# Optimization experiments

Measured on AMD Instinct MI355X. Metric: run time of the kernel, lower is better.

The kernel has to match this reference:

```python
import jax, jax.numpy as jnp
import numpy as np
import math

B, T, V, D, H = 64, 128, 25, 256, 8
HD = D // H  # head_dim = 32
LN_EPS = 1e-5
NORM_EPS = 1e-12  # F.normalize default eps


def _layernorm(x, g, b):
    m = jnp.mean(x, axis=-1, keepdims=True)
    v = jnp.mean(jnp.square(x - m), axis=-1, keepdims=True)
    return (x - m) * jax.lax.rsqrt(v + LN_EPS) * g + b


def setup_inputs() -> dict:
    key = jax.random.key(0)
    ks = jax.random.split(key, 10)
    s = 0.02
    return {
        "x": jax.random.normal(ks[0], (B, T, V, D), dtype=jnp.float32),
        "ln1_g": jnp.ones((D,), jnp.float32),
        "ln1_b": jnp.zeros((D,), jnp.float32),
        "qkv_w": jax.random.normal(ks[1], (D, 3 * D), jnp.float32) * s,
        "qkv_b": jnp.zeros((3 * D,), jnp.float32),
        "proj_w": jax.random.normal(ks[2], (D, D), jnp.float32) * s,
        "proj_b": jnp.zeros((D,), jnp.float32),
        "logit_scale": jnp.full((H, 1, 1), math.log(math.sqrt(HD)), jnp.float32),
        "ln2_g": jnp.ones((D,), jnp.float32),
        "ln2_b": jnp.zeros((D,), jnp.float32),
        "ffn_w1": jax.random.normal(ks[3], (D, 4 * D), jnp.float32) * s,
        "ffn_b1": jnp.zeros((4 * D,), jnp.float32),
        "ffn_w2": jax.random.normal(ks[4], (4 * D, D), jnp.float32) * s,
        "ffn_b2": jnp.zeros((D,), jnp.float32),
    }


def reference(x, ln1_g, ln1_b, qkv_w, qkv_b, proj_w, proj_b, logit_scale,
              ln2_g, ln2_b, ffn_w1, ffn_b1, ffn_w2, ffn_b2):
    b, t, v, dm = x.shape
    n = b * t
    h, d = H, HD
    xf = x.reshape(n, v, dm)
    residual = xf
    y = _layernorm(xf, ln1_g, ln1_b)
    qkv = (y @ qkv_w + qkv_b).reshape(n, v, 3, h, d)
    qkv = jnp.transpose(qkv, (2, 0, 3, 1, 4))  # (3, n, h, v, d)
    q, k, val = qkv[0], qkv[1], qkv[2]
    # cosine attention: L2-normalize q/k, learned per-head temperature (clamped at 100)
    scale = jnp.exp(jnp.minimum(logit_scale, math.log(100.0)))  # (h,1,1)
    q = q / jnp.maximum(jnp.linalg.norm(q, axis=-1, keepdims=True), NORM_EPS) * scale[None]
    k = k / jnp.maximum(jnp.linalg.norm(k, axis=-1, keepdims=True), NORM_EPS)
    # SDPA applies its default 1/sqrt(head_dim) scaling on top
    logits = jnp.einsum('nhqd,nhkd->nhqk', q, k) / math.sqrt(d)
    attn = jax.nn.softmax(logits, axis=-1)
    out = jnp.einsum('nhqk,nhkd->nhqd', attn, val)
    out = jnp.transpose(out, (0, 2, 1, 3)).reshape(n, v, dm)
    out = out @ proj_w + proj_b
    xf = residual + out
    y2 = _layernorm(xf, ln2_g, ln2_b)
    ffn = jax.nn.gelu(y2 @ ffn_w1 + ffn_b1, approximate=False) @ ffn_w2 + ffn_b2
    xf = xf + ffn
    return xf.reshape(b, t, v, dm)
```

## Files before the change

### kernel.cpp

```cpp
#include <hip/hip_runtime.h>
#include <stdint.h>

typedef unsigned short u16;
typedef __attribute__((ext_vector_type(8))) short short8;
typedef __attribute__((ext_vector_type(4))) float f32x4;

__device__ __forceinline__ float bf2f(u16 v) {
  union { uint32_t u; float f; } x; x.u = ((uint32_t)v) << 16; return x.f;
}
__device__ __forceinline__ u16 f2bf(float f) {
  union { float f; uint32_t u; } x; x.f = f;
  uint32_t u = x.u;
  return (u16)((u + 0x7fffu + ((u >> 16) & 1u)) >> 16);
}
__device__ __forceinline__ void unp8(int4 r, float* f) {
  f[0] = __uint_as_float(((uint32_t)r.x) << 16);
  f[1] = __uint_as_float(((uint32_t)r.x) & 0xffff0000u);
  f[2] = __uint_as_float(((uint32_t)r.y) << 16);
  f[3] = __uint_as_float(((uint32_t)r.y) & 0xffff0000u);
  f[4] = __uint_as_float(((uint32_t)r.z) << 16);
  f[5] = __uint_as_float(((uint32_t)r.z) & 0xffff0000u);
  f[6] = __uint_as_float(((uint32_t)r.w) << 16);
  f[7] = __uint_as_float(((uint32_t)r.w) & 0xffff0000u);
}

__device__ __forceinline__ void copy16(const u16* g, u16* l) {
#if defined(__has_builtin) && __has_builtin(__builtin_amdgcn_global_load_lds)
  uintptr_t li = (uintptr_t)l;
  uintptr_t gi = (uintptr_t)g;
  __builtin_amdgcn_global_load_lds((const __attribute__((address_space(1))) uint32_t*)gi,
                                   (__attribute__((address_space(3))) uint32_t*)li, 16, 0, 0);
#else
  *(int4*)l = *(const int4*)g;
#endif
}

__global__ __launch_bounds__(256) void k0_prep(const float* __restrict__ qkvw,
                                               const float* __restrict__ projw,
                                               const float* __restrict__ w1,
                                               const float* __restrict__ w2,
                                               u16* __restrict__ wbuf) {
  int idx = blockIdx.x * 256 + threadIdx.x;
  if (idx < 196608) {
    int nn = idx >> 8, kk = idx & 255;
    wbuf[idx] = f2bf(qkvw[kk * 768 + nn]);
  } else if (idx < 262144) {
    int i = idx - 196608; int nn = i >> 8, kk = i & 255;
    wbuf[idx] = f2bf(projw[kk * 256 + nn]);
  } else if (idx < 524288) {
    int i = idx - 262144; int nn = i >> 8, kk = i & 255;
    wbuf[idx] = f2bf(w1[kk * 1024 + nn]);
  } else {
    int i = idx - 524288; int nn = i >> 10, kk = i & 1023;
    wbuf[idx] = f2bf(w2[kk * 256 + nn]);
  }
}

__global__ __launch_bounds__(256) void k1_ln1(const float* __restrict__ x,
                                              const float* __restrict__ g,
                                              const float* __restrict__ b,
                                              u16* __restrict__ Y, int row0) {
  int t = threadIdx.x; int lr = t >> 6; int lane = t & 63;
  size_t row = (size_t)blockIdx.x * 4 + lr;
  const float4 xv = *(const float4*)&x[((size_t)row0 + row) * 256 + lane * 4];
  float s = xv.x + xv.y + xv.z + xv.w;
  float q = xv.x * xv.x + xv.y * xv.y + xv.z * xv.z + xv.w * xv.w;
  #pragma unroll
  for (int off = 32; off > 0; off >>= 1) { s += __shfl_xor(s, off); q += __shfl_xor(q, off); }
  float mean = s * (1.0f / 256.0f);
  float var  = q * (1.0f / 256.0f) - mean * mean;
  float rstd = rsqrtf(var + 1e-5f);
  const float4 gv = *(const float4*)&g[lane * 4];
  const float4 bv = *(const float4*)&b[lane * 4];
  float y0 = (xv.x - mean) * rstd * gv.x + bv.x;
  float y1 = (xv.y - mean) * rstd * gv.y + bv.y;
  float y2 = (xv.z - mean) * rstd * gv.z + bv.z;
  float y3 = (xv.w - mean) * rstd * gv.w + bv.w;
  uint2 r;
  r.x = (uint32_t)f2bf(y0) | ((uint32_t)f2bf(y1) << 16);
  r.y = (uint32_t)f2bf(y2) | ((uint32_t)f2bf(y3) << 16);
  *(uint2*)&Y[row * 256 + lane * 4] = r;
}

template <int NB, bool GELU>
__global__ __launch_bounds__(256) void kA_gemm(const u16* __restrict__ A, const u16* __restrict__ Bw,
                                               const float* __restrict__ bias, u16* __restrict__ C) {
  __shared__ u16 Al[64 * 264];
  __shared__ u16 Bl[128 * 32];
  const int t = threadIdx.x, w = t >> 6, lane = t & 63, quad = lane >> 4, lrow = lane & 15;
  const int wm = w >> 1, wn = w & 1;
  const int mb = blockIdx.x * 64;
  #pragma unroll
  for (int r = 0; r < 8; r++) {
    int c = r * 256 + t;
    int row = c >> 5, col = (c & 31) * 8;
    int4 v = *(const int4*)&A[(size_t)(mb + row) * 256 + col];
    *(int4*)&Al[row * 264 + col] = v;
  }
  constexpr int LDC = NB * 128;
  for (int nb = 0; nb < NB; nb++) {
    f32x4 acc[2][4];
    #pragma unroll
    for (int i = 0; i < 2; i++)
      #pragma unroll
      for (int j = 0; j < 4; j++) acc[i][j] = f32x4{0.f, 0.f, 0.f, 0.f};
    for (int kc = 0; kc < 8; kc++) {
      #pragma unroll
      for (int r = 0; r < 2; r++) {
        int c = r * 256 + w * 64 + lane;
        u16* lp = Bl + (size_t)(r * 256 + w * 64) * 8;
        const u16* gp = Bw + (size_t)(nb * 128 + (c >> 2)) * 256 + kc * 32 + (c & 3) * 8;
        copy16(gp, lp);
      }
      __syncthreads();
      short8 af[2], bfr[4];
      #pragma unroll
      for (int mt = 0; mt < 2; mt++)
        af[mt] = *(const short8*)&Al[(wm * 32 + mt * 16 + lrow) * 264 + kc * 32 + quad * 8];
      #pragma unroll
      for (int nt = 0; nt < 4; nt++)
        bfr[nt] = *(const short8*)&Bl[(wn * 64 + nt * 16 + lrow) * 32 + quad * 8];
      #pragma unroll
      for (int mt = 0; mt < 2; mt++)
        #pragma unroll
        for (int nt = 0; nt < 4; nt++)
          acc[mt][nt] = __builtin_amdgcn_mfma_f32_16x16x32_bf16(af[mt], bfr[nt], acc[mt][nt], 0, 0, 0);
      __syncthreads();
    }
    #pragma unroll
    for (int nt = 0; nt < 4; nt++) {
      int n = nb * 128 + wn * 64 + nt * 16 + lrow;
      float bv = bias[n];
      #pragma unroll
      for (int mt = 0; mt < 2; mt++)
        #pragma unroll
        for (int i = 0; i < 4; i++) {
          int m = mb + wm * 32 + mt * 16 + quad * 4 + i;
          float u = acc[mt][nt][i] + bv;
          if (GELU) u = 0.5f * u * (1.0f + erff(u * 0.70710678118654752440f));
          C[(size_t)m * LDC + n] = f2bf(u);
        }
    }
  }
}

__global__ __launch_bounds__(256) void k3_attn(const u16* __restrict__ QKV,
                                               const float* __restrict__ lscale,
                                               u16* __restrict__ O) {
  __shared__ u16 Kl[8192];
  __shared__ u16 Vt[10304];
  __shared__ u16 Pl[4][1280];
  __shared__ float invk[256];

  const int n = blockIdx.x;
  const int t = threadIdx.x;
  const int w = t >> 6, lane = t & 63, quad = lane >> 4, l15 = lane & 15;
  const size_t n25 = (size_t)n * 25;

  #pragma unroll
  for (int r = 0; r < 4; r++) {
    int c = r * 256 + t;
    if (c < 800) {
      int vr = c >> 5, ci = c & 31;
      const u16* gp = QKV + (n25 + vr) * 768 + 256 + (size_t)((ci ^ (vr & 7)) * 8);
      u16* lp = Kl + (size_t)(r * 256 + w * 64) * 8;
      copy16(gp, lp);
    }
  }
  #pragma unroll
  for (int r = 0; r < 4; r++) {
    int c = r * 256 + t;
    if (c < 800) {
      int vr = c >> 5, ci = c & 31, h = ci >> 2, d8 = (ci & 3) * 8;
      int4 rv = *(const int4*)&QKV[(n25 + vr) * 768 + 512 + ci * 8];
      int base = h * 1288 + d8 * 40 + vr;
      Vt[base +   0] = (u16)((uint32_t)rv.x & 0xffffu);
      Vt[base +  40] = (u16)((uint32_t)rv.x >> 16);
      Vt[base +  80] = (u16)((uint32_t)rv.y & 0xffffu);
      Vt[base + 120] = (u16)((uint32_t)rv.y >> 16);
      Vt[base + 160] = (u16)((uint32_t)rv.z & 0xffffu);
      Vt[base + 200] = (u16)((uint32_t)rv.z >> 16);
      Vt[base + 240] = (u16)((uint32_t)rv.w & 0xffffu);
      Vt[base + 280] = (u16)((uint32_t)rv.w >> 16);
    }
  }
  {
    int h = t >> 5, d = t & 31;
    int base = h * 1288 + d * 40 + 25;
    #pragma unroll
    for (int j = 0; j < 7; j++) Vt[base + j] = 0;
  }
  __syncthreads();

  if (t < 200) {
    int h = (t * 41) >> 10;
    int vr = t - h * 25;
    float ss = 0.f;
    #pragma unroll
    for (int q = 0; q < 4; q++) {
      int chunk = (h * 4 + q) ^ (vr & 7);
      int4 rv = *(const int4*)&Kl[vr * 256 + chunk * 8];
      float f[8]; unp8(rv, f);
      #pragma unroll
      for (int j = 0; j < 8; j++) ss += f[j] * f[j];
    }
    invk[h * 32 + vr] = 1.0f / fmaxf(sqrtf(ss), 1e-12f);
  } else {
    int u = t - 200;
    int h = (u * 37) >> 8;
    int j = u - h * 7;
    invk[h * 32 + 25 + j] = 0.f;
  }
  __syncthreads();

  const u16* qbase = QKV + n25 * 768;
  const f32x4 zz = {0.f, 0.f, 0.f, 0.f};
  #pragma unroll
  for (int hh = 0; hh < 2; hh++) {
    const int h = w * 2 + hh;
    const float sc = expf(fminf(lscale[h], 4.6051701859880913680f));

    short8 af0 = *(const short8*)(qbase + (size_t)l15 * 768 + h * 32 + quad * 8);
    short8 af1 = *(const short8*)(qbase + (size_t)(16 + l15) * 768 + h * 32 + quad * 8);
    short8 bf0 = *(const short8*)&Kl[l15 * 256 + (((h * 4 + quad) ^ (l15 & 7)) * 8)];
    short8 bf1 = *(const short8*)&Kl[(16 + l15) * 256 + (((h * 4 + quad) ^ ((16 + l15) & 7)) * 8)];
    f32x4 sA[2][2];
    sA[0][0] = __builtin_amdgcn_mfma_f32_16x16x32_bf16(af0, bf0, zz, 0, 0, 0);
    sA[0][1] = __builtin_amdgcn_mfma_f32_16x16x32_bf16(af0, bf1, zz, 0, 0, 0);
    sA[1][0] = __builtin_amdgcn_mfma_f32_16x16x32_bf16(af1, bf0, zz, 0, 0, 0);
    sA[1][1] = __builtin_amdgcn_mfma_f32_16x16x32_bf16(af1, bf1, zz, 0, 0, 0);

    float ss0 = 0.f, ss1 = 0.f;
    #pragma unroll
    for (int j = 0; j < 8; j++) {
      float f0 = bf2f((u16)af0[j]); ss0 += f0 * f0;
      float f1 = bf2f((u16)af1[j]); ss1 += f1 * f1;
    }
    ss0 += __shfl_xor(ss0, 16); ss0 += __shfl_xor(ss0, 32);
    ss1 += __shfl_xor(ss1, 16); ss1 += __shfl_xor(ss1, 32);
    float fct0 = sc / (fmaxf(sqrtf(ss0), 1e-12f) * 5.6568542494923802f);
    float fct1 = sc / (fmaxf(sqrtf(ss1), 1e-12f) * 5.6568542494923802f);

    const float ik0 = invk[h * 32 + l15];
    const float ik1 = invk[h * 32 + 16 + l15];
    const bool v1 = l15 < 9;

    #pragma unroll
    for (int qt = 0; qt < 2; qt++) {
      #pragma unroll
      for (int i = 0; i < 4; i++) {
        float fr = __shfl(qt == 0 ? fct0 : fct1, quad * 4 + i);
        float l0 = sA[qt][0][i] * fr * ik0;
        float l1 = sA[qt][1][i] * fr * ik1;
        float m = fmaxf(l0, v1 ? l1 : -1e30f);
        #pragma unroll
        for (int o = 1; o < 16; o <<= 1) m = fmaxf(m, __shfl_xor(m, o));
        float e0 = expf(l0 - m);
        float e1 = v1 ? expf(l1 - m) : 0.f;
        float se = e0 + e1;
        #pragma unroll
        for (int o = 1; o < 16; o <<= 1) se += __shfl_xor(se, o);
        float inv = 1.0f / se;
        int q = qt * 16 + quad * 4 + i;
        Pl[w][q * 40 + l15]      = f2bf(e0 * inv);
        Pl[w][q * 40 + 16 + l15] = f2bf(e1 * inv);
      }
    }

    short8 pa0 = *(const short8*)&Pl[w][l15 * 40 + quad * 8];
    short8 pa1 = *(const short8*)&Pl[w][(16 + l15) * 40 + quad * 8];
    short8 vb0 = *(const short8*)&Vt[h * 1288 + l15 * 40 + quad * 8];
    short8 vb1 = *(const short8*)&Vt[h * 1288 + (16 + l15) * 40 + quad * 8];
    f32x4 oA[2][2];
    oA[0][0] = __builtin_amdgcn_mfma_f32_16x16x32_bf16(pa0, vb0, zz, 0, 0, 0);
    oA[0][1] = __builtin_amdgcn_mfma_f32_16x16x32_bf16(pa0, vb1, zz, 0, 0, 0);
    oA[1][0] = __builtin_amdgcn_mfma_f32_16x16x32_bf16(pa1, vb0, zz, 0, 0, 0);
    oA[1][1] = __builtin_amdgcn_mfma_f32_16x16x32_bf16(pa1, vb1, zz, 0, 0, 0);

    u16* ob = O + n25 * 256 + h * 32;
    #pragma unroll
    for (int qt = 0; qt < 2; qt++)
      #pragma unroll
      for (int i = 0; i < 4; i++) {
        int qr = quad * 4 + i;
        if (qt == 1 && qr >= 9) continue;
        int q = qt * 16 + qr;
        ob[(size_t)q * 256 + l15]      = f2bf(oA[qt][0][i]);
        ob[(size_t)q * 256 + 16 + l15] = f2bf(oA[qt][1][i]);
      }
  }
}

template <int BM, int BN>
__device__ __forceinline__ void gemm_core(const u16* __restrict__ A, const u16* __restrict__ Bw,
                                          int K, int mbase, int nbase, u16* lds, f32x4 acc[4][4]) {
  const int t = threadIdx.x;
  const int w = t >> 6, lane = t & 63, quad = lane >> 4, lrow = lane & 15;
  constexpr int WN = BN / 64;
  const int wm = w / WN, wn = w % WN;
  u16* pA = lds;
  u16* pB = lds + BM * 32;
  #pragma unroll
  for (int i = 0; i < 4; i++)
    #pragma unroll
    for (int j = 0; j < 4; j++) acc[i][j] = f32x4{0.f, 0.f, 0.f, 0.f};
  constexpr int ROUNDS = (BM + BN) / 64;
  for (int k0 = 0; k0 < K; k0 += 32) {
    #pragma unroll
    for (int q = 0; q < ROUNDS; q++) {
      int c = q * 256 + w * 64 + lane;
      u16* lp = lds + (size_t)(q * 256 + w * 64) * 8;
      const u16* gp;
      if (c < BM * 4) {
        gp = A + (size_t)(mbase + (c >> 2)) * (size_t)K + k0 + (c & 3) * 8;
      } else {
        int cb = c - BM * 4;
        gp = Bw + (size_t)(nbase + (cb >> 2)) * (size_t)K + k0 + (cb & 3) * 8;
      }
      copy16(gp, lp);
    }
    __syncthreads();
    short8 af[4], bfr[4];
    #pragma unroll
    for (int mt = 0; mt < 4; mt++)
      af[mt] = *(const short8*)(pA + (size_t)(wm * 64 + mt * 16 + lrow) * 32 + quad * 8);
    #pragma unroll
    for (int nt = 0; nt < 4; nt++)
      bfr[nt] = *(const short8*)(pB + (size_t)(wn * 64 + nt * 16 + lrow) * 32 + quad * 8);
    #pragma unroll
    for (int mt = 0; mt < 4; mt++)
      #pragma unroll
      for (int nt = 0; nt < 4; nt++)
        acc[mt][nt] = __builtin_amdgcn_mfma_f32_16x16x32_bf16(af[mt], bfr[nt], acc[mt][nt], 0, 0, 0);
    __syncthreads();
  }
}

__global__ __launch_bounds__(256) void k4_proj(const u16* __restrict__ A, const u16* __restrict__ Bw,
                                               const float* __restrict__ bias,
                                               const float* __restrict__ x,
                                               const float* __restrict__ g2, const float* __restrict__ b2,
                                               u16* __restrict__ xfb, u16* __restrict__ y2b, int row0) {
  __shared__ u16 lds[10240];
  __shared__ float ps[4][64], pq[4][64], meanv[64], rstdv[64];
  f32x4 acc[4][4];
  const int mb = blockIdx.x * 64;
  gemm_core<64, 256>(A, Bw, 256, mb, 0, lds, acc);
  const int t = threadIdx.x, w = t >> 6, lane = t & 63, quad = lane >> 4, lrow = lane & 15;
  const int wn = w;
  #pragma unroll
  for (int nt = 0; nt < 4; nt++) {
    int nn = wn * 64 + nt * 16 + lrow;
    float bv = bias[nn];
    #pragma unroll
    for (int mt = 0; mt < 4; mt++)
      #pragma unroll
      for (int i = 0; i < 4; i++) {
        int m = mb + mt * 16 + quad * 4 + i;
        acc[mt][nt][i] += bv + x[((size_t)row0 + m) * 256 + nn];
      }
  }
  #pragma unroll
  for (int mt = 0; mt < 4; mt++)
    #pragma unroll
    for (int i = 0; i < 4; i++) {
      float s = 0.f, q = 0.f;
      #pragma unroll
      for (int nt = 0; nt < 4; nt++) { float v = acc[mt][nt][i]; s += v; q += v * v; }
      #pragma unroll
      for (int off = 1; off < 16; off <<= 1) { s += __shfl_xor(s, off); q += __shfl_xor(q, off); }
      if (lrow == 0) { int r = mt * 16 + quad * 4 + i; ps[w][r] = s; pq[w][r] = q; }
    }
  __syncthreads();
  if (t < 64) {
    float s = ps[0][t] + ps[1][t] + ps[2][t] + ps[3][t];
    float q = pq[0][t] + pq[1][t] + pq[2][t] + pq[3][t];
    float mean = s * (1.0f / 256.0f);
    float var  = q * (1.0f / 256.0f) - mean * mean;
    meanv[t] = mean; rstdv[t] = rsqrtf(var + 1e-5f);
  }
  __syncthreads();
  #pragma unroll
  for (int nt = 0; nt < 4; nt++) {
    int nn = wn * 64 + nt * 16 + lrow;
    float gg = g2[nn], bb = b2[nn];
    #pragma unroll
    for (int mt = 0; mt < 4; mt++)
      #pragma unroll
      for (int i = 0; i < 4; i++) {
        int r = mt * 16 + quad * 4 + i;
        int m = mb + r;
        float xfv = acc[mt][nt][i];
        xfb[(size_t)m * 256 + nn] = f2bf(xfv);
        y2b[(size_t)m * 256 + nn] = f2bf((xfv - meanv[r]) * rstdv[r] * gg + bb);
      }
  }
}

__global__ __launch_bounds__(256) void k6_ffn2(const u16* __restrict__ G, const u16* __restrict__ W2w,
                                               const float* __restrict__ bias,
                                               const u16* __restrict__ xfb,
                                               float* __restrict__ out, int row0) {
  __shared__ u16 Al[64 * 264];
  __shared__ u16 Bl[256 * 32];
  const int t = threadIdx.x, w = t >> 6, lane = t & 63, quad = lane >> 4, lrow = lane & 15;
  const int wn = w;
  const int mb = blockIdx.x * 64;
  f32x4 acc[4][4];
  #pragma unroll
  for (int i = 0; i < 4; i++)
    #pragma unroll
    for (int j = 0; j < 4; j++) acc[i][j] = f32x4{0.f, 0.f, 0.f, 0.f};
  for (int kch = 0; kch < 4; kch++) {
    #pragma unroll
    for (int r = 0; r < 8; r++) {
      int c = r * 256 + t;
      int row = c >> 5, col = (c & 31) * 8;
      int4 v = *(const int4*)&G[(size_t)(mb + row) * 1024 + kch * 256 + col];
      *(int4*)&Al[row * 264 + col] = v;
    }
    for (int kc = 0; kc < 8; kc++) {
      #pragma unroll
      for (int r = 0; r < 4; r++) {
        int c = r * 256 + w * 64 + lane;
        u16* lp = Bl + (size_t)(r * 256 + w * 64) * 8;
        const u16* gp = W2w + (size_t)(c >> 2) * 1024 + kch * 256 + kc * 32 + (c & 3) * 8;
        copy16(gp, lp);
      }
      __syncthreads();
      short8 af[4], bfr[4];
      #pragma unroll
      for (int mt = 0; mt < 4; mt++)
        af[mt] = *(const short8*)&Al[(mt * 16 + lrow) * 264 + kc * 32 + quad * 8];
      #pragma unroll
      for (int nt = 0; nt < 4; nt++)
        bfr[nt] = *(const short8*)&Bl[(wn * 64 + nt * 16 + lrow) * 32 + quad * 8];
      #pragma unroll
      for (int mt = 0; mt < 4; mt++)
        #pragma unroll
        for (int nt = 0; nt < 4; nt++)
          acc[mt][nt] = __builtin_amdgcn_mfma_f32_16x16x32_bf16(af[mt], bfr[nt], acc[mt][nt], 0, 0, 0);
      __syncthreads();
    }
  }
  #pragma unroll
  for (int nt = 0; nt < 4; nt++) {
    int n = wn * 64 + nt * 16 + lrow;
    float bv = bias[n];
    #pragma unroll
    for (int mt = 0; mt < 4; mt++)
      #pragma unroll
      for (int i = 0; i < 4; i++) {
        int m = mb + mt * 16 + quad * 4 + i;
        out[((size_t)row0 + m) * 256 + n] = acc[mt][nt][i] + bv + bf2f(xfb[(size_t)m * 256 + n]);
      }
  }
}

#define WEIGHT_BYTES 1572864ull

extern "C" void kernel_launch(void* const* d_in, const int* in_sizes, int n_in,
                              void* d_out, int out_size, void* d_ws, size_t ws_size,
                              hipStream_t stream) {
  const float* x     = (const float*)d_in[0];
  const float* ln1g  = (const float*)d_in[1];
  const float* ln1b  = (const float*)d_in[2];
  const float* qkvw  = (const float*)d_in[3];
  const float* qkvb  = (const float*)d_in[4];
  const float* projw = (const float*)d_in[5];
  const float* projb = (const float*)d_in[6];
  const float* lsc   = (const float*)d_in[7];
  const float* ln2g  = (const float*)d_in[8];
  const float* ln2b  = (const float*)d_in[9];
  const float* w1    = (const float*)d_in[10];
  const float* b1    = (const float*)d_in[11];
  const float* w2    = (const float*)d_in[12];
  const float* b2    = (const float*)d_in[13];
  float* out = (float*)d_out;
  char* wsb = (char*)d_ws;

  u16* wbuf = (u16*)wsb;
  u16* WQ = wbuf;
  u16* WP = wbuf + 196608;
  u16* W1 = wbuf + 262144;
  u16* W2 = wbuf + 524288;

  size_t avail = ws_size > WEIGHT_BYTES ? ws_size - WEIGHT_BYTES : 0;
  int nchunks = 64;
  for (int c = 1; c <= 64; c <<= 1) {
    size_t Rr = 204800u / (unsigned)c;
    if (Rr * 5632ull <= avail) { nchunks = c; break; }
  }
  const int R = 204800 / nchunks;
  char* cb = wsb + WEIGHT_BYTES;
  u16* Ybuf = (u16*)(cb);
  u16* QKVb = (u16*)(cb + (size_t)R * 512);
  u16* Obuf = (u16*)(cb + (size_t)R * 2048);
  u16* XFb  = (u16*)(cb + (size_t)R * 2560);
  u16* Y2b  = (u16*)(cb + (size_t)R * 3072);
  u16* Gbuf = (u16*)(cb + (size_t)R * 3584);

  k0_prep<<<3072, 256, 0, stream>>>(qkvw, projw, w1, w2, wbuf);
  for (int c = 0; c < nchunks; c++) {
    int row0 = c * R;
    k1_ln1<<<R / 4, 256, 0, stream>>>(x, ln1g, ln1b, Ybuf, row0);
    kA_gemm<6, false><<<R / 64, 256, 0, stream>>>(Ybuf, WQ, qkvb, QKVb);
    k3_attn<<<R / 25, 256, 0, stream>>>(QKVb, lsc, Obuf);
    k4_proj<<<R / 64, 256, 0, stream>>>(Obuf, WP, projb, x, ln2g, ln2b, XFb, Y2b, row0);
    kA_gemm<8, true><<<R / 64, 256, 0, stream>>>(Y2b, W1, b1, Gbuf);
    k6_ffn2<<<R / 64, 256, 0, stream>>>(Gbuf, W2, b2, XFb, out, row0);
  }
}
```

Measured before the change: 1.606 ms.

## Load GEMM weight fragments directly from global memory, drop LDS staging and barriers

In the QKV/FFN1, projection and FFN2 GEMM kernels, weight (B) fragments are now read straight from global memory into registers instead of being staged through shared memory each k-step. This removes the per-iteration LDS copy and the two __syncthreads barriers inside the k loop. The projection kernel also stages its whole 64x256 activation tile in LDS once, replacing the shared gemm_core. In exchange, each wave issues its own uncoalesced 16-byte global loads for weights, relying on L1/L2 caching. There is no software prefetch, so memory latency may be exposed directly before the MFMAs.

```diff
diff --git a/kernel.cpp b/kernel.cpp
--- a/kernel.cpp
+++ b/kernel.cpp
@@ -86,7 +86,6 @@
 __global__ __launch_bounds__(256) void kA_gemm(const u16* __restrict__ A, const u16* __restrict__ Bw,
                                                const float* __restrict__ bias, u16* __restrict__ C) {
   __shared__ u16 Al[64 * 264];
-  __shared__ u16 Bl[128 * 32];
   const int t = threadIdx.x, w = t >> 6, lane = t & 63, quad = lane >> 4, lrow = lane & 15;
   const int wm = w >> 1, wn = w & 1;
   const int mb = blockIdx.x * 64;
@@ -97,6 +96,7 @@
     int4 v = *(const int4*)&A[(size_t)(mb + row) * 256 + col];
     *(int4*)&Al[row * 264 + col] = v;
   }
+  __syncthreads();
   constexpr int LDC = NB * 128;
   for (int nb = 0; nb < NB; nb++) {
     f32x4 acc[2][4];
@@ -105,27 +105,18 @@
       #pragma unroll
       for (int j = 0; j < 4; j++) acc[i][j] = f32x4{0.f, 0.f, 0.f, 0.f};
     for (int kc = 0; kc < 8; kc++) {
-      #pragma unroll
-      for (int r = 0; r < 2; r++) {
-        int c = r * 256 + w * 64 + lane;
-        u16* lp = Bl + (size_t)(r * 256 + w * 64) * 8;
-        const u16* gp = Bw + (size_t)(nb * 128 + (c >> 2)) * 256 + kc * 32 + (c & 3) * 8;
-        copy16(gp, lp);
-      }
-      __syncthreads();
       short8 af[2], bfr[4];
+      #pragma unroll
+      for (int nt = 0; nt < 4; nt++)
+        bfr[nt] = *(const short8*)&Bw[(size_t)(nb * 128 + wn * 64 + nt * 16 + lrow) * 256 + kc * 32 + quad * 8];
       #pragma unroll
       for (int mt = 0; mt < 2; mt++)
         af[mt] = *(const short8*)&Al[(wm * 32 + mt * 16 + lrow) * 264 + kc * 32 + quad * 8];
-      #pragma unroll
-      for (int nt = 0; nt < 4; nt++)
-        bfr[nt] = *(const short8*)&Bl[(wn * 64 + nt * 16 + lrow) * 32 + quad * 8];
       #pragma unroll
       for (int mt = 0; mt < 2; mt++)
         #pragma unroll
         for (int nt = 0; nt < 4; nt++)
           acc[mt][nt] = __builtin_amdgcn_mfma_f32_16x16x32_bf16(af[mt], bfr[nt], acc[mt][nt], 0, 0, 0);
-      __syncthreads();
     }
     #pragma unroll
     for (int nt = 0; nt < 4; nt++) {
@@ -291,63 +282,43 @@
   }
 }
 
-template <int BM, int BN>
-__device__ __forceinline__ void gemm_core(const u16* __restrict__ A, const u16* __restrict__ Bw,
-                                          int K, int mbase, int nbase, u16* lds, f32x4 acc[4][4]) {
-  const int t = threadIdx.x;
-  const int w = t >> 6, lane = t & 63, quad = lane >> 4, lrow = lane & 15;
-  constexpr int WN = BN / 64;
-  const int wm = w / WN, wn = w % WN;
-  u16* pA = lds;
-  u16* pB = lds + BM * 32;
-  #pragma unroll
-  for (int i = 0; i < 4; i++)
-    #pragma unroll
-    for (int j = 0; j < 4; j++) acc[i][j] = f32x4{0.f, 0.f, 0.f, 0.f};
-  constexpr int ROUNDS = (BM + BN) / 64;
-  for (int k0 = 0; k0 < K; k0 += 32) {
-    #pragma unroll
-    for (int q = 0; q < ROUNDS; q++) {
-      int c = q * 256 + w * 64 + lane;
-      u16* lp = lds + (size_t)(q * 256 + w * 64) * 8;
-      const u16* gp;
-      if (c < BM * 4) {
-        gp = A + (size_t)(mbase + (c >> 2)) * (size_t)K + k0 + (c & 3) * 8;
-      } else {
-        int cb = c - BM * 4;
-        gp = Bw + (size_t)(nbase + (cb >> 2)) * (size_t)K + k0 + (cb & 3) * 8;
-      }
-      copy16(gp, lp);
-    }
-    __syncthreads();
-    short8 af[4], bfr[4];
-    #pragma unroll
-    for (int mt = 0; mt < 4; mt++)
-      af[mt] = *(const short8*)(pA + (size_t)(wm * 64 + mt * 16 + lrow) * 32 + quad * 8);
-    #pragma unroll
-    for (int nt = 0; nt < 4; nt++)
-      bfr[nt] = *(const short8*)(pB + (size_t)(wn * 64 + nt * 16 + lrow) * 32 + quad * 8);
-    #pragma unroll
-    for (int mt = 0; mt < 4; mt++)
-      #pragma unroll
-      for (int nt = 0; nt < 4; nt++)
-        acc[mt][nt] = __builtin_amdgcn_mfma_f32_16x16x32_bf16(af[mt], bfr[nt], acc[mt][nt], 0, 0, 0);
-    __syncthreads();
-  }
-}
-
 __global__ __launch_bounds__(256) void k4_proj(const u16* __restrict__ A, const u16* __restrict__ Bw,
                                                const float* __restrict__ bias,
                                                const float* __restrict__ x,
                                                const float* __restrict__ g2, const float* __restrict__ b2,
                                                u16* __restrict__ xfb, u16* __restrict__ y2b, int row0) {
-  __shared__ u16 lds[10240];
+  __shared__ u16 Al[64 * 264];
   __shared__ float ps[4][64], pq[4][64], meanv[64], rstdv[64];
-  f32x4 acc[4][4];
-  const int mb = blockIdx.x * 64;
-  gemm_core<64, 256>(A, Bw, 256, mb, 0, lds, acc);
   const int t = threadIdx.x, w = t >> 6, lane = t & 63, quad = lane >> 4, lrow = lane & 15;
   const int wn = w;
+  const int mb = blockIdx.x * 64;
+  #pragma unroll
+  for (int r = 0; r < 8; r++) {
+    int c = r * 256 + t;
+    int row = c >> 5, col = (c & 31) * 8;
+    int4 v = *(const int4*)&A[(size_t)(mb + row) * 256 + col];
+    *(int4*)&Al[row * 264 + col] = v;
+  }
+  __syncthreads();
+  f32x4 acc[4][4];
+  #pragma unroll
+  for (int i = 0; i < 4; i++)
+    #pragma unroll
+    for (int j = 0; j < 4; j++) acc[i][j] = f32x4{0.f, 0.f, 0.f, 0.f};
+  for (int kc = 0; kc < 8; kc++) {
+    short8 af[4], bfr[4];
+    #pragma unroll
+    for (int nt = 0; nt < 4; nt++)
+      bfr[nt] = *(const short8*)&Bw[(size_t)(wn * 64 + nt * 16 + lrow) * 256 + kc * 32 + quad * 8];
+    #pragma unroll
+    for (int mt = 0; mt < 4; mt++)
+      af[mt] = *(const short8*)&Al[(mt * 16 + lrow) * 264 + kc * 32 + quad * 8];
+    #pragma unroll
+    for (int mt = 0; mt < 4; mt++)
+      #pragma unroll
+      for (int nt = 0; nt < 4; nt++)
+        acc[mt][nt] = __builtin_amdgcn_mfma_f32_16x16x32_bf16(af[mt], bfr[nt], acc[mt][nt], 0, 0, 0);
+  }
   #pragma unroll
   for (int nt = 0; nt < 4; nt++) {
     int nn = wn * 64 + nt * 16 + lrow;
@@ -402,7 +373,6 @@
                                                const u16* __restrict__ xfb,
                                                float* __restrict__ out, int row0) {
   __shared__ u16 Al[64 * 264];
-  __shared__ u16 Bl[256 * 32];
   const int t = threadIdx.x, w = t >> 6, lane = t & 63, quad = lane >> 4, lrow = lane & 15;
   const int wn = w;
   const int mb = blockIdx.x * 64;
@@ -412,6 +382,7 @@
     #pragma unroll
     for (int j = 0; j < 4; j++) acc[i][j] = f32x4{0.f, 0.f, 0.f, 0.f};
   for (int kch = 0; kch < 4; kch++) {
+    __syncthreads();
     #pragma unroll
     for (int r = 0; r < 8; r++) {
       int c = r * 256 + t;
@@ -419,28 +390,20 @@
       int4 v = *(const int4*)&G[(size_t)(mb + row) * 1024 + kch * 256 + col];
       *(int4*)&Al[row * 264 + col] = v;
     }
+    __syncthreads();
     for (int kc = 0; kc < 8; kc++) {
-      #pragma unroll
-      for (int r = 0; r < 4; r++) {
-        int c = r * 256 + w * 64 + lane;
-        u16* lp = Bl + (size_t)(r * 256 + w * 64) * 8;
-        const u16* gp = W2w + (size_t)(c >> 2) * 1024 + kch * 256 + kc * 32 + (c & 3) * 8;
-        copy16(gp, lp);
-      }
-      __syncthreads();
       short8 af[4], bfr[4];
+      #pragma unroll
+      for (int nt = 0; nt < 4; nt++)
+        bfr[nt] = *(const short8*)&W2w[(size_t)(wn * 64 + nt * 16 + lrow) * 1024 + kch * 256 + kc * 32 + quad * 8];
       #pragma unroll
       for (int mt = 0; mt < 4; mt++)
         af[mt] = *(const short8*)&Al[(mt * 16 + lrow) * 264 + kc * 32 + quad * 8];
-      #pragma unroll
-      for (int nt = 0; nt < 4; nt++)
-        bfr[nt] = *(const short8*)&Bl[(wn * 64 + nt * 16 + lrow) * 32 + quad * 8];
       #pragma unroll
       for (int mt = 0; mt < 4; mt++)
         #pragma unroll
         for (int nt = 0; nt < 4; nt++)
           acc[mt][nt] = __builtin_amdgcn_mfma_f32_16x16x32_bf16(af[mt], bfr[nt], acc[mt][nt], 0, 0, 0);
-      __syncthreads();
     }
   }
   #pragma unroll
```

Measured after the change: 1.940 ms. 1.21x slower.
